# Optimization experiments

Measured on AMD Instinct MI355X. Metric: run time of the kernel, lower is better.

The kernel has to match this reference:

```python
import jax, jax.numpy as jnp
import numpy as np

D_MODEL = 1024
N_HEADS = 16
HEAD_DIM = D_MODEL // N_HEADS  # 64, rope_dim == head_dim
D_FF = 4096
BATCH = 2
SEQ = 2048
EPS = 1e-6


def setup_inputs() -> dict:
    key = jax.random.key(0)
    ks = jax.random.split(key, 12)
    x = jax.random.normal(ks[0], (BATCH, SEQ, D_MODEL), dtype=jnp.float32)
    # realistic RoPE angles: theta = pos * inv_freq, duplicated to fill rope_dim
    half = HEAD_DIM // 2
    inv_freq = 1.0 / (10000.0 ** (jnp.arange(0, half, dtype=jnp.float32) / half))
    pos = jnp.arange(SEQ, dtype=jnp.float32)
    freqs = pos[:, None] * inv_freq[None, :]              # [S, half]
    rotary_pos_emb = jnp.concatenate([freqs, freqs], axis=-1)[:, None, :]  # [S,1,64]
    s = D_MODEL ** -0.5
    wq = jax.random.normal(ks[1], (D_MODEL, D_MODEL), dtype=jnp.float32) * s
    wk = jax.random.normal(ks[2], (D_MODEL, D_MODEL), dtype=jnp.float32) * s
    wv = jax.random.normal(ks[3], (D_MODEL, D_MODEL), dtype=jnp.float32) * s
    wo = jax.random.normal(ks[4], (D_MODEL, D_MODEL), dtype=jnp.float32) * s
    w_gate = jax.random.normal(ks[5], (D_FF, D_MODEL), dtype=jnp.float32) * s
    w_up = jax.random.normal(ks[6], (D_FF, D_MODEL), dtype=jnp.float32) * s
    w_down = jax.random.normal(ks[7], (D_MODEL, D_FF), dtype=jnp.float32) * (D_FF ** -0.5)
    norm1_w = jnp.ones((D_MODEL,), dtype=jnp.float32)
    norm2_w = jnp.ones((D_MODEL,), dtype=jnp.float32)
    return {"x": x, "rotary_pos_emb": rotary_pos_emb, "wq": wq, "wk": wk,
            "wv": wv, "wo": wo, "w_gate": w_gate, "w_up": w_up,
            "w_down": w_down, "norm1_w": norm1_w, "norm2_w": norm2_w}


def _rms_norm(x, w):
    # torch: x / (||x||/sqrt(d) + eps) * w  (eps added to the norm, not variance)
    norm = jnp.linalg.norm(x, axis=-1, keepdims=True) * (x.shape[-1] ** -0.5)
    return x / (norm + EPS) * w


def _rotate_half(t):
    t1, t2 = jnp.split(t, 2, axis=-1)
    return jnp.concatenate([-t2, t1], axis=-1)


def _apply_rope(t, cos, sin):
    # t: [B,H,S,D]; cos/sin: [S,D] broadcast over batch/heads
    return t * cos[None, None] + _rotate_half(t) * sin[None, None]


def reference(x, rotary_pos_emb, wq, wk, wv, wo, w_gate, w_up, w_down, norm1_w, norm2_w):
    B, S, _ = x.shape
    H, D = N_HEADS, HEAD_DIM

    # ---- attention sublayer ----
    residual = x
    h = _rms_norm(x, norm1_w)
    q = (h @ wq.T).reshape(B, S, H, D).transpose(0, 2, 1, 3)  # [B,H,S,D]
    k = (h @ wk.T).reshape(B, S, H, D).transpose(0, 2, 1, 3)
    v = (h @ wv.T).reshape(B, S, H, D).transpose(0, 2, 1, 3)

    freqs = rotary_pos_emb[:, 0, :]  # [S, D] (rope_dim == head_dim)
    cos, sin = jnp.cos(freqs), jnp.sin(freqs)
    q = _apply_rope(q, cos, sin)
    k = _apply_rope(k, cos, sin)

    scores = jnp.einsum('bhsd,bhtd->bhst', q, k) / jnp.sqrt(jnp.float32(D))
    causal = jnp.tril(jnp.ones((S, S), dtype=bool))  # True = keep
    scores = jnp.where(causal[None, None], scores, jnp.finfo(scores.dtype).min)
    attn = jax.nn.softmax(scores, axis=-1)  # dropout is identity in eval
    attn_out = jnp.einsum('bhst,bhtd->bhsd', attn, v)
    attn_out = attn_out.transpose(0, 2, 1, 3).reshape(B, S, H * D)
    x = residual + attn_out @ wo.T

    # ---- SwiGLU MLP sublayer ----
    residual = x
    h = _rms_norm(x, norm2_w)
    gate = h @ w_gate.T
    up = h @ w_up.T
    ff = (jax.nn.silu(gate) * up) @ w_down.T
    return residual + ff
```

## Files before the change

### kernel.cpp

```cpp
#include <hip/hip_runtime.h>

typedef __bf16 bf16;
typedef __attribute__((ext_vector_type(8))) __bf16 bf16x8;
typedef __attribute__((ext_vector_type(4))) float f32x4;

#define B_SZ 2
#define SEQ 2048
#define DM 1024
#define NH 16
#define HD 64
#define DFF 4096
#define NROWS (B_SZ*SEQ)

__device__ __forceinline__ f32x4 mfma16(bf16x8 a, bf16x8 b, f32x4 c) {
    return __builtin_amdgcn_mfma_f32_16x16x32_bf16(a, b, c, 0, 0, 0);
}

__device__ __forceinline__ void gload16(const bf16* g, bf16* l) {
    __builtin_amdgcn_global_load_lds(
        (const __attribute__((address_space(1))) void*)g,
        (__attribute__((address_space(3))) void*)l, 16, 0, 0);
}


__global__ __launch_bounds__(256) void f32_to_bf16_k(const float* __restrict__ s,
                                                     bf16* __restrict__ d, int n) {
    int i = (blockIdx.x * 256 + threadIdx.x) * 4;
    int stride = gridDim.x * 1024;
    for (; i < n; i += stride) {
        float4 v = *(const float4*)(s + i);
        d[i]   = (bf16)v.x; d[i+1] = (bf16)v.y;
        d[i+2] = (bf16)v.z; d[i+3] = (bf16)v.w;
    }
}

__global__ __launch_bounds__(256) void conv_gu_k(const float* __restrict__ g,
                                                 const float* __restrict__ u,
                                                 bf16* __restrict__ d) {
    int i = (blockIdx.x * 256 + threadIdx.x) * 4;
    int fr = i >> 10, c = i & 1023;
    int b = fr >> 8, half = (fr >> 7) & 1, f = (b << 7) | (fr & 127);
    const float* src = (half ? u : g) + (long)f * 1024 + c;
    float4 v = *(const float4*)src;
    d[i]   = (bf16)v.x; d[i+1] = (bf16)v.y;
    d[i+2] = (bf16)v.z; d[i+3] = (bf16)v.w;
}

__global__ __launch_bounds__(256) void rope_table_k(const float* __restrict__ rope,
                                                    float* __restrict__ ct,
                                                    float* __restrict__ st) {
    int i = blockIdx.x * 256 + threadIdx.x;
    int sI = i >> 5, d = i & 31;
    float f = rope[sI * 64 + d];
    ct[i] = cosf(f);
    st[i] = sinf(f);
}

__global__ __launch_bounds__(256) void rmsnorm_k(const float* __restrict__ x,
                                                 const float* __restrict__ w,
                                                 bf16* __restrict__ o) {
    int row = blockIdx.x;
    int tid = threadIdx.x;
    float4 v = ((const float4*)(x + (long)row * DM))[tid];
    float ss = v.x*v.x + v.y*v.y + v.z*v.z + v.w*v.w;
    #pragma unroll
    for (int off = 32; off >= 1; off >>= 1) ss += __shfl_xor(ss, off, 64);
    __shared__ float sred[4];
    if ((tid & 63) == 0) sred[tid >> 6] = ss;
    __syncthreads();
    float tot = sred[0] + sred[1] + sred[2] + sred[3];
    float scale = 1.f / (sqrtf(tot * (1.f / (float)DM)) + 1e-6f);
    float4 wv = ((const float4*)w)[tid];
    bf16* orow = o + (long)row * DM + tid * 4;
    orow[0] = (bf16)(v.x * scale * wv.x);
    orow[1] = (bf16)(v.y * scale * wv.y);
    orow[2] = (bf16)(v.z * scale * wv.z);
    orow[3] = (bf16)(v.w * scale * wv.w);
}


template<int EPI>
__global__ __launch_bounds__(512, 2)
void gemm256(const bf16* __restrict__ A, const bf16* __restrict__ W,
             int K, bf16* __restrict__ o1, bf16* __restrict__ o2,
             bf16* __restrict__ o3,
             const float* __restrict__ ct, const float* __restrict__ st) {
    __shared__ __align__(16) char smem[131072];
    const int tid = threadIdx.x;
    const int wid = tid >> 6, l = tid & 63;
    const int lr = l & 15, lg = l >> 4;
    const int wr = wid >> 1, wc = wid & 1;
    const int nwg = gridDim.x * gridDim.y;
    const int orig = blockIdx.y * gridDim.x + blockIdx.x;
    const int swz = (orig & 7) * (nwg >> 3) + (orig >> 3);
    const int bx = swz % gridDim.x, by = swz / gridDim.x;
    const long mbase = (long)bx * 256;
    const long nbase = (long)by * 256;

    f32x4 acc[4][8] = {};
    const int nk = K >> 6;

    auto stage = [&](int b, int kt) {
        bf16* bufA = (bf16*)(smem + b * 65536);
        bf16* bufB = (bf16*)(smem + b * 65536 + 32768);
        #pragma unroll
        for (int i = 0; i < 4; ++i) {
            int s = i * 512 + tid;
            int row = s >> 3, c8 = (s & 7) << 3;
            gload16(&A[(mbase + row) * K + kt * 64 + c8], bufA + s * 8);
            gload16(&W[(nbase + row) * K + kt * 64 + c8], bufB + s * 8);
        }
    };
    auto compute = [&](int b) {
        const bf16* bufA = (const bf16*)(smem + b * 65536);
        const bf16* bufB = (const bf16*)(smem + b * 65536 + 32768);
        #pragma unroll
        for (int kk = 0; kk < 2; ++kk) {
            bf16x8 af[4], bfr[8];
            #pragma unroll
            for (int mi = 0; mi < 4; ++mi)
                af[mi] = *(const bf16x8*)&bufA[(wr * 64 + mi * 16 + lr) * 64 + kk * 32 + lg * 8];
            #pragma unroll
            for (int ni = 0; ni < 8; ++ni)
                bfr[ni] = *(const bf16x8*)&bufB[(wc * 128 + ni * 16 + lr) * 64 + kk * 32 + lg * 8];
            #pragma unroll
            for (int mi = 0; mi < 4; ++mi)
                #pragma unroll
                for (int ni = 0; ni < 8; ++ni)
                    acc[mi][ni] = mfma16(af[mi], bfr[ni], acc[mi][ni]);
        }
    };

    stage(0, 0);
    __syncthreads();
    int cur = 0;
    for (int kt = 0; kt < nk - 1; ++kt) {
        stage(cur ^ 1, kt + 1);
        compute(cur);
        __syncthreads();
        cur ^= 1;
    }
    compute(cur);

    if (EPI == 0) {
        const long colW = nbase + wc * 128;
        const int sect = (int)(colW >> 10);
        #pragma unroll
        for (int mi = 0; mi < 4; ++mi) {
            #pragma unroll
            for (int nn = 0; nn < 4; ++nn) {
                const int ni = (nn & 1) + (nn >> 1) * 4;
                const int col = (int)colW + ni * 16 + lr;
                const int h = (col >> 6) & 15;
                const int d = col & 31;
                #pragma unroll
                for (int r = 0; r < 4; ++r) {
                    long row = mbase + wr * 64 + mi * 16 + 4 * lg + r;
                    int b = (int)(row >> 11), s = (int)(row & 2047);
                    float v1 = acc[mi][ni][r];
                    float v2 = acc[mi][ni + 2][r];
                    if (sect < 2) {
                        float c = ct[s * 32 + d], sn = st[s * 32 + d];
                        bf16* dst = (sect == 0) ? o1 : o2;
                        long p = (((long)(b * NH + h) * SEQ + s) << 6) + d;
                        dst[p]      = (bf16)(v1 * c - v2 * sn);
                        dst[p + 32] = (bf16)(v2 * c + v1 * sn);
                    } else {
                        long p = ((long)(b * NH + h) * HD + d) * SEQ + s;
                        o3[p]            = (bf16)v1;
                        o3[p + 32 * SEQ] = (bf16)v2;
                    }
                }
            }
        }
    }

    if (EPI == 3) {
        const int fbase = (int)(nbase >> 1);
        bf16* Gl = (bf16*)smem;
        __syncthreads();
        if (wc == 0) {
            #pragma unroll
            for (int mi = 0; mi < 4; ++mi)
                #pragma unroll
                for (int ni = 0; ni < 8; ++ni)
                    #pragma unroll
                    for (int r = 0; r < 4; ++r) {
                        int grow = wr * 64 + mi * 16 + 4 * lg + r;
                        Gl[grow * 132 + ni * 16 + lr] = (bf16)acc[mi][ni][r];
                    }
        }
        __syncthreads();
        if (wc == 1) {
            #pragma unroll
            for (int mi = 0; mi < 4; ++mi)
                #pragma unroll
                for (int ni = 0; ni < 8; ++ni)
                    #pragma unroll
                    for (int r = 0; r < 4; ++r) {
                        int grow = wr * 64 + mi * 16 + 4 * lg + r;
                        float g = (float)Gl[grow * 132 + ni * 16 + lr];
                        float u = acc[mi][ni][r];
                        float sg = g / (1.f + __expf(-g));
                        long row = mbase + grow;
                        o1[row * 4096 + fbase + ni * 16 + lr] = (bf16)(sg * u);
                    }
        }
    }
}


__global__ __launch_bounds__(512, 4)
void gemm64x128(const bf16* __restrict__ A, const bf16* __restrict__ W,
                int K, int N, const float* __restrict__ resid, float* __restrict__ of) {
    __shared__ bf16 As[2][64 * 64];
    __shared__ bf16 Bs[2][128 * 64];
    const int tid = threadIdx.x;
    const int wid = tid >> 6, l = tid & 63;
    const int lr = l & 15, lg = l >> 4;
    const int wr = wid >> 2, wcn = wid & 3;
    const long mbase = (long)blockIdx.x * 64;
    const long nbase = (long)blockIdx.y * 128;

    f32x4 acc[2][2] = {};
    const int nk = K >> 6;

    auto stage = [&](int b, int kt) {
        {
            int s = tid;
            int row = s >> 3, c8 = (s & 7) << 3;
            gload16(&A[(mbase + row) * K + kt * 64 + c8], &As[b][s * 8]);
        }
        #pragma unroll
        for (int i = 0; i < 2; ++i) {
            int s = i * 512 + tid;
            int row = s >> 3, c8 = (s & 7) << 3;
            gload16(&W[(nbase + row) * K + kt * 64 + c8], &Bs[b][s * 8]);
        }
    };
    auto compute = [&](int b) {
        #pragma unroll
        for (int kk = 0; kk < 2; ++kk) {
            bf16x8 af[2], bfr[2];
            #pragma unroll
            for (int mi = 0; mi < 2; ++mi)
                af[mi] = *(const bf16x8*)&As[b][(wr * 32 + mi * 16 + lr) * 64 + kk * 32 + lg * 8];
            #pragma unroll
            for (int ni = 0; ni < 2; ++ni)
                bfr[ni] = *(const bf16x8*)&Bs[b][(wcn * 32 + ni * 16 + lr) * 64 + kk * 32 + lg * 8];
            #pragma unroll
            for (int mi = 0; mi < 2; ++mi)
                #pragma unroll
                for (int ni = 0; ni < 2; ++ni)
                    acc[mi][ni] = mfma16(af[mi], bfr[ni], acc[mi][ni]);
        }
    };

    stage(0, 0);
    __syncthreads();
    int cur = 0;
    for (int kt = 0; kt < nk - 1; ++kt) {
        stage(cur ^ 1, kt + 1);
        compute(cur);
        __syncthreads();
        cur ^= 1;
    }
    compute(cur);

    #pragma unroll
    for (int mi = 0; mi < 2; ++mi)
        #pragma unroll
        for (int ni = 0; ni < 2; ++ni)
            #pragma unroll
            for (int r = 0; r < 4; ++r) {
                long row = mbase + wr * 32 + mi * 16 + 4 * lg + r;
                long col = nbase + wcn * 32 + ni * 16 + lr;
                of[row * N + col] = resid[row * N + col] + acc[mi][ni][r];
            }
}


__device__ __forceinline__ void attn_tile(
    int tb, int qw, bool diag,
    const bf16x8& qf0, const bf16x8& qf1,
    const bf16* Kl, const bf16* Vl, bf16* Plw,
    int lr, int lg, f32x4* oacc, float* mr, f32x4& lacc)
{
    f32x4 s[4];
    __builtin_amdgcn_s_setprio(1);
    #pragma unroll
    for (int tf = 0; tf < 4; ++tf) {
        f32x4 z = {0.f, 0.f, 0.f, 0.f};
        bf16x8 k0 = *(const bf16x8*)&Kl[(tf * 16 + lr) * 64 + ((0 + lg) ^ (lr & 7)) * 8];
        bf16x8 k1 = *(const bf16x8*)&Kl[(tf * 16 + lr) * 64 + ((4 + lg) ^ (lr & 7)) * 8];
        z = mfma16(qf0, k0, z);
        z = mfma16(qf1, k1, z);
        s[tf] = z;
    }
    __builtin_amdgcn_s_setprio(0);

    float pv[4][4];
    float pmax[4] = {-1e30f, -1e30f, -1e30f, -1e30f};
    #pragma unroll
    for (int tf = 0; tf < 4; ++tf) {
        int t = tb + tf * 16 + lr;
        #pragma unroll
        for (int r = 0; r < 4; ++r) {
            float sv = s[tf][r] * 0.125f;
            if (diag && t > qw + 4 * lg + r) sv = -1e30f;
            pv[tf][r] = sv;
            pmax[r] = fmaxf(pmax[r], sv);
        }
    }
    #pragma unroll
    for (int r = 0; r < 4; ++r) {
        pmax[r] = fmaxf(pmax[r], __shfl_xor(pmax[r], 8, 64));
        pmax[r] = fmaxf(pmax[r], __shfl_xor(pmax[r], 4, 64));
        pmax[r] = fmaxf(pmax[r], __shfl_xor(pmax[r], 2, 64));
        pmax[r] = fmaxf(pmax[r], __shfl_xor(pmax[r], 1, 64));
    }
    float alpha[4];
    #pragma unroll
    for (int r = 0; r < 4; ++r) {
        float mn = fmaxf(mr[r], pmax[r]);
        alpha[r] = __expf(mr[r] - mn);
        mr[r] = mn;
    }
    #pragma unroll
    for (int tf = 0; tf < 4; ++tf)
        #pragma unroll
        for (int r = 0; r < 4; ++r)
            Plw[(4 * lg + r) * 68 + tf * 16 + lr] = (bf16)__expf(pv[tf][r] - mr[r]);

    #pragma unroll
    for (int r = 0; r < 4; ++r) lacc[r] *= alpha[r];
    #pragma unroll
    for (int df = 0; df < 4; ++df) {
        f32x4 t4 = oacc[df];
        t4[0] *= alpha[0]; t4[1] *= alpha[1];
        t4[2] *= alpha[2]; t4[3] *= alpha[3];
        oacc[df] = t4;
    }
    bf16x8 pa0, pa1;
    #pragma unroll
    for (int j = 0; j < 8; ++j) {
        pa0[j] = Plw[lr * 68 + lg * 8 + j];
        pa1[j] = Plw[lr * 68 + 32 + lg * 8 + j];
    }
    bf16x8 ones;
    #pragma unroll
    for (int j = 0; j < 8; ++j) ones[j] = (bf16)1.0f;
    __builtin_amdgcn_s_setprio(1);
    lacc = mfma16(pa0, ones, lacc);
    lacc = mfma16(pa1, ones, lacc);
    #pragma unroll
    for (int df = 0; df < 4; ++df) {
        bf16x8 v0 = *(const bf16x8*)&Vl[(df * 16 + lr) * 64 + ((0 + lg) ^ (lr & 7)) * 8];
        bf16x8 v1 = *(const bf16x8*)&Vl[(df * 16 + lr) * 64 + ((4 + lg) ^ (lr & 7)) * 8];
        oacc[df] = mfma16(pa0, v0, oacc[df]);
        oacc[df] = mfma16(pa1, v1, oacc[df]);
    }
    __builtin_amdgcn_s_setprio(0);
}

__global__ __launch_bounds__(256)
void attn_fwd(const bf16* __restrict__ q, const bf16* __restrict__ k,
              const bf16* __restrict__ vt, bf16* __restrict__ o) {
    __shared__ bf16 Kl[2][64 * 64];
    __shared__ bf16 Vl[2][64 * 64];
    __shared__ bf16 Pl[4][16 * 68];
    const int tid = threadIdx.x, wid = tid >> 6, l = tid & 63;
    const int lr = l & 15, lg = l >> 4;
    const int qtA = blockIdx.x;
    const int qtB = 31 - qtA;
    const int bh = blockIdx.y;
    const long kbase = (long)bh * SEQ * HD;
    const long vbase = (long)bh * HD * SEQ;
    const int qwA = qtA * 64 + wid * 16;
    const int qwB = qtB * 64 + wid * 16;

    bf16x8 qA0, qA1, qB0, qB1;
    {
        const bf16* qp = q + kbase + (long)(qwA + lr) * HD + lg * 8;
        qA0 = *(const bf16x8*)qp; qA1 = *(const bf16x8*)(qp + 32);
        const bf16* qp2 = q + kbase + (long)(qwB + lr) * HD + lg * 8;
        qB0 = *(const bf16x8*)qp2; qB1 = *(const bf16x8*)(qp2 + 32);
    }
    f32x4 oA[4] = {}, oB[4] = {};
    f32x4 lA = {0.f, 0.f, 0.f, 0.f}, lB = {0.f, 0.f, 0.f, 0.f};
    float mA[4] = {-1e30f, -1e30f, -1e30f, -1e30f};
    float mB[4] = {-1e30f, -1e30f, -1e30f, -1e30f};

    auto stageKV = [&](int b, int tb) {
        #pragma unroll
        for (int i = 0; i < 4; ++i) {
            int slot = i * 256 + tid;
            int row = (slot >> 3) & 63;
            int bs = (slot & 7) ^ (row & 7);
            if (slot < 512)
                gload16(&k[kbase + (long)(tb + row) * HD + bs * 8], &Kl[b][slot * 8]);
            else
                gload16(&vt[vbase + (long)row * SEQ + tb + bs * 8], &Vl[b][(slot - 512) * 8]);
        }
    };

    const int nt = qtB + 1;
    stageKV(0, 0);
    __syncthreads();
    int cur = 0;
    for (int tb_i = 0; tb_i < nt; ++tb_i) {
        const int tb = tb_i * 64;
        if (tb_i + 1 < nt) stageKV(cur ^ 1, tb + 64);
        if (tb_i <= qtA)
            attn_tile(tb, qwA, tb_i == qtA, qA0, qA1, Kl[cur], Vl[cur], Pl[wid], lr, lg, oA, mA, lA);
        attn_tile(tb, qwB, tb_i == qtB, qB0, qB1, Kl[cur], Vl[cur], Pl[wid], lr, lg, oB, mB, lB);
        __syncthreads();
        cur ^= 1;
    }

    const int b = bh >> 4, h = bh & 15;
    #pragma unroll
    for (int df = 0; df < 4; ++df) {
        #pragma unroll
        for (int r = 0; r < 4; ++r) {
            int sA = qwA + 4 * lg + r;
            int sB = qwB + 4 * lg + r;
            o[((long)(b * SEQ + sA) * DM) + h * HD + df * 16 + lr] = (bf16)(oA[df][r] / lA[r]);
            o[((long)(b * SEQ + sB) * DM) + h * HD + df * 16 + lr] = (bf16)(oB[df][r] / lB[r]);
        }
    }
}


extern "C" void kernel_launch(void* const* d_in, const int* in_sizes, int n_in,
                              void* d_out, int out_size, void* d_ws, size_t ws_size,
                              hipStream_t stream) {
    (void)in_sizes; (void)n_in; (void)out_size; (void)ws_size;
    const float* x    = (const float*)d_in[0];
    const float* rope = (const float*)d_in[1];
    const float* wq   = (const float*)d_in[2];
    const float* wk   = (const float*)d_in[3];
    const float* wv   = (const float*)d_in[4];
    const float* wo   = (const float*)d_in[5];
    const float* wg   = (const float*)d_in[6];
    const float* wu   = (const float*)d_in[7];
    const float* wd   = (const float*)d_in[8];
    const float* n1w  = (const float*)d_in[9];
    const float* n2w  = (const float*)d_in[10];
    float* out = (float*)d_out;

    char* ws = (char*)d_ws;
    const size_t MB = 1u << 20;
    bf16* wqkvb = (bf16*)(ws + 0 * MB);
    bf16* wob   = (bf16*)(ws + 6 * MB);
    bf16* wgub  = (bf16*)(ws + 8 * MB);
    bf16* wdb   = (bf16*)(ws + 24 * MB);
    bf16* hb    = (bf16*)(ws + 32 * MB);
    bf16* qb_   = (bf16*)(ws + 40 * MB);
    bf16* kb_   = (bf16*)(ws + 56 * MB);
    bf16* vtb   = (bf16*)(ws + 72 * MB);
    bf16* attnb = (bf16*)(ws + 88 * MB);
    float* x2   = (float*)(ws + 40 * MB);
    bf16* midb  = (bf16*)(ws + 56 * MB);
    float* ctab = (float*)(ws + 104 * MB);
    float* stab = (float*)(ws + 104 * MB + (1u << 18));

    f32_to_bf16_k<<<1024, 256, 0, stream>>>(wq, wqkvb,               DM * DM);
    f32_to_bf16_k<<<1024, 256, 0, stream>>>(wk, wqkvb + 1024 * 1024, DM * DM);
    f32_to_bf16_k<<<1024, 256, 0, stream>>>(wv, wqkvb + 2048 * 1024, DM * DM);
    f32_to_bf16_k<<<1024, 256, 0, stream>>>(wo, wob, DM * DM);
    conv_gu_k<<<8192, 256, 0, stream>>>(wg, wu, wgub);
    f32_to_bf16_k<<<2048, 256, 0, stream>>>(wd, wdb, DM * DFF);
    rope_table_k<<<256, 256, 0, stream>>>(rope, ctab, stab);

    rmsnorm_k<<<NROWS, 256, 0, stream>>>(x, n1w, hb);

    gemm256<0><<<dim3(16, 12), 512, 0, stream>>>(hb, wqkvb, DM, qb_, kb_, vtb, ctab, stab);

    attn_fwd<<<dim3(16, 32), 256, 0, stream>>>(qb_, kb_, vtb, attnb);

    gemm64x128<<<dim3(64, 8), 512, 0, stream>>>(attnb, wob, DM, DM, x, x2);

    rmsnorm_k<<<NROWS, 256, 0, stream>>>(x2, n2w, hb);

    gemm256<3><<<dim3(16, 32), 512, 0, stream>>>(hb, wgub, DM, midb, nullptr, nullptr, nullptr, nullptr);

    gemm64x128<<<dim3(64, 8), 512, 0, stream>>>(midb, wdb, DFF, DM, x2, out);
}
```

Before: 353.8 us.

## Fuse weight conversions and deepen gemm256 pipeline with swizzled half-K stages

Merges six weight-conversion launches into one kernel that converts eight elements per thread. Reworks the 256x256 GEMM to stage half K-tiles (32 columns) into a four-deep ring in LDS with an XOR swizzle. It waits on explicit vmcnt counts plus a raw s_barrier instead of __syncthreads, and raises wave priority around the MFMA bursts. The warp layout changes from 4x2 to 2x4 waves, so the RoPE and SwiGLU epilogues are remapped. This aims to hide load latency and cut LDS bank conflicts, at the cost of fragile hand-written wait counts and synchronisation.

```diff
diff --git a/kernel.cpp b/kernel.cpp
--- a/kernel.cpp
+++ b/kernel.cpp
@@ -23,27 +23,34 @@
 }
 
 
-__global__ __launch_bounds__(256) void f32_to_bf16_k(const float* __restrict__ s,
-                                                     bf16* __restrict__ d, int n) {
-    int i = (blockIdx.x * 256 + threadIdx.x) * 4;
-    int stride = gridDim.x * 1024;
-    for (; i < n; i += stride) {
-        float4 v = *(const float4*)(s + i);
-        d[i]   = (bf16)v.x; d[i+1] = (bf16)v.y;
-        d[i+2] = (bf16)v.z; d[i+3] = (bf16)v.w;
-    }
-}
-
-__global__ __launch_bounds__(256) void conv_gu_k(const float* __restrict__ g,
-                                                 const float* __restrict__ u,
-                                                 bf16* __restrict__ d) {
-    int i = (blockIdx.x * 256 + threadIdx.x) * 4;
-    int fr = i >> 10, c = i & 1023;
-    int b = fr >> 8, half = (fr >> 7) & 1, f = (b << 7) | (fr & 127);
-    const float* src = (half ? u : g) + (long)f * 1024 + c;
-    float4 v = *(const float4*)src;
-    d[i]   = (bf16)v.x; d[i+1] = (bf16)v.y;
-    d[i+2] = (bf16)v.z; d[i+3] = (bf16)v.w;
+__global__ __launch_bounds__(256) void convert_all_k(
+    const float* __restrict__ wq, const float* __restrict__ wk,
+    const float* __restrict__ wv, const float* __restrict__ wo,
+    const float* __restrict__ wg, const float* __restrict__ wu,
+    const float* __restrict__ wd,
+    bf16* __restrict__ wqkvb, bf16* __restrict__ wob,
+    bf16* __restrict__ wgub, bf16* __restrict__ wdb) {
+    const long M1 = 1l << 20;
+    long i = ((long)blockIdx.x * 256 + threadIdx.x) * 8;
+    const float* src; bf16* dst; long off;
+    if (i < 3 * M1) {
+        int sct = (int)(i >> 20);
+        src = sct == 0 ? wq : (sct == 1 ? wk : wv);
+        off = i & (M1 - 1); dst = wqkvb + i;
+    } else if (i < 4 * M1) {
+        src = wo; off = i - 3 * M1; dst = wob + off;
+    } else if (i < 12 * M1) {
+        long j = i - 4 * M1;
+        int fr = (int)(j >> 10), c = (int)(j & 1023);
+        int b = fr >> 8, half = (fr >> 7) & 1, f = (b << 7) | (fr & 127);
+        src = half ? wu : wg; off = (long)f * 1024 + c; dst = wgub + j;
+    } else {
+        src = wd; off = i - 12 * M1; dst = wdb + off;
+    }
+    float4 v0 = *(const float4*)(src + off);
+    float4 v1 = *(const float4*)(src + off + 4);
+    dst[0] = (bf16)v0.x; dst[1] = (bf16)v0.y; dst[2] = (bf16)v0.z; dst[3] = (bf16)v0.w;
+    dst[4] = (bf16)v1.x; dst[5] = (bf16)v1.y; dst[6] = (bf16)v1.z; dst[7] = (bf16)v1.w;
 }
 
 __global__ __launch_bounds__(256) void rope_table_k(const float* __restrict__ rope,
@@ -86,10 +93,12 @@
              bf16* __restrict__ o3,
              const float* __restrict__ ct, const float* __restrict__ st) {
     __shared__ __align__(16) char smem[131072];
+    bf16* Ah = (bf16*)smem;
+    bf16* Bh = (bf16*)(smem + 65536);
     const int tid = threadIdx.x;
     const int wid = tid >> 6, l = tid & 63;
     const int lr = l & 15, lg = l >> 4;
-    const int wr = wid >> 1, wc = wid & 1;
+    const int wr = wid >> 2, wcn = wid & 3;
     const int nwg = gridDim.x * gridDim.y;
     const int orig = blockIdx.y * gridDim.x + blockIdx.x;
     const int swz = (orig & 7) * (nwg >> 3) + (orig >> 3);
@@ -97,78 +106,91 @@
     const long mbase = (long)bx * 256;
     const long nbase = (long)by * 256;
 
-    f32x4 acc[4][8] = {};
+    f32x4 acc[8][4] = {};
     const int nk = K >> 6;
-
-    auto stage = [&](int b, int kt) {
-        bf16* bufA = (bf16*)(smem + b * 65536);
-        bf16* bufB = (bf16*)(smem + b * 65536 + 32768);
-        #pragma unroll
-        for (int i = 0; i < 4; ++i) {
+    const int P = nk * 2;
+
+    const int aoff0 = lr * 64 + ((wr * 4 + lg) ^ (lr & 7)) * 8;
+    const int boff0 = ((wcn & 1) * 64 + lr) * 64 + (((wcn >> 1) * 4 + lg) ^ (lr & 7)) * 8;
+
+    auto stageHalf = [&](int ph) {
+        const int d = (ph >> 1) & 1, h = ph & 1, kt = ph >> 1;
+        bf16* abase = Ah + (d * 2 + h) * 8192;
+        bf16* bbase = Bh + (d * 2 + h) * 8192;
+        const long kcol = (long)kt * 64 + h * 32;
+        #pragma unroll
+        for (int i = 0; i < 2; ++i) {
             int s = i * 512 + tid;
-            int row = s >> 3, c8 = (s & 7) << 3;
-            gload16(&A[(mbase + row) * K + kt * 64 + c8], bufA + s * 8);
-            gload16(&W[(nbase + row) * K + kt * 64 + c8], bufB + s * 8);
+            int prow = s >> 3, pblk = s & 7;
+            int L = pblk ^ (prow & 7);
+            long gr = (long)((L >> 2) * 128 + prow);
+            long gc = kcol + (L & 3) * 8;
+            gload16(&A[(mbase + gr) * K + gc], abase + s * 8);
+            gload16(&W[(nbase + gr) * K + gc], bbase + s * 8);
         }
     };
-    auto compute = [&](int b) {
-        const bf16* bufA = (const bf16*)(smem + b * 65536);
-        const bf16* bufB = (const bf16*)(smem + b * 65536 + 32768);
-        #pragma unroll
-        for (int kk = 0; kk < 2; ++kk) {
-            bf16x8 af[4], bfr[8];
+
+    auto computeHalf = [&](int ph) {
+        const int d = (ph >> 1) & 1, h = ph & 1;
+        const bf16* abase = Ah + (d * 2 + h) * 8192;
+        const bf16* bbase = Bh + (d * 2 + h) * 8192;
+        bf16x8 bfr[4];
+        #pragma unroll
+        for (int ni = 0; ni < 4; ++ni)
+            bfr[ni] = *(const bf16x8*)&bbase[ni * 1024 + boff0];
+        #pragma unroll
+        for (int ms = 0; ms < 2; ++ms) {
+            bf16x8 af[4];
             #pragma unroll
             for (int mi = 0; mi < 4; ++mi)
-                af[mi] = *(const bf16x8*)&bufA[(wr * 64 + mi * 16 + lr) * 64 + kk * 32 + lg * 8];
-            #pragma unroll
-            for (int ni = 0; ni < 8; ++ni)
-                bfr[ni] = *(const bf16x8*)&bufB[(wc * 128 + ni * 16 + lr) * 64 + kk * 32 + lg * 8];
+                af[mi] = *(const bf16x8*)&abase[(ms * 4 + mi) * 1024 + aoff0];
+            __builtin_amdgcn_s_setprio(1);
             #pragma unroll
             for (int mi = 0; mi < 4; ++mi)
                 #pragma unroll
-                for (int ni = 0; ni < 8; ++ni)
-                    acc[mi][ni] = mfma16(af[mi], bfr[ni], acc[mi][ni]);
+                for (int ni = 0; ni < 4; ++ni)
+                    acc[ms * 4 + mi][ni] = mfma16(af[mi], bfr[ni], acc[ms * 4 + mi][ni]);
+            __builtin_amdgcn_s_setprio(0);
         }
     };
 
-    stage(0, 0);
-    __syncthreads();
-    int cur = 0;
-    for (int kt = 0; kt < nk - 1; ++kt) {
-        stage(cur ^ 1, kt + 1);
-        compute(cur);
-        __syncthreads();
-        cur ^= 1;
-    }
-    compute(cur);
+    stageHalf(0);
+    stageHalf(1);
+    for (int p = 0; p < P; ++p) {
+        if (p + 2 < P) stageHalf(p + 2);
+        if (p < P - 2)       asm volatile("s_waitcnt vmcnt(8)" ::: "memory");
+        else if (p == P - 2) asm volatile("s_waitcnt vmcnt(4)" ::: "memory");
+        else                 asm volatile("s_waitcnt vmcnt(0)" ::: "memory");
+        __builtin_amdgcn_s_barrier();
+        __builtin_amdgcn_sched_barrier(0);
+        computeHalf(p);
+    }
 
     if (EPI == 0) {
-        const long colW = nbase + wc * 128;
+        const long colW = nbase + wcn * 64;
         const int sect = (int)(colW >> 10);
-        #pragma unroll
-        for (int mi = 0; mi < 4; ++mi) {
-            #pragma unroll
-            for (int nn = 0; nn < 4; ++nn) {
-                const int ni = (nn & 1) + (nn >> 1) * 4;
-                const int col = (int)colW + ni * 16 + lr;
-                const int h = (col >> 6) & 15;
-                const int d = col & 31;
+        const int hh = (int)((colW >> 6) & 15);
+        #pragma unroll
+        for (int a = 0; a < 8; ++a) {
+            #pragma unroll
+            for (int nn = 0; nn < 2; ++nn) {
+                const int dd = nn * 16 + lr;
                 #pragma unroll
                 for (int r = 0; r < 4; ++r) {
-                    long row = mbase + wr * 64 + mi * 16 + 4 * lg + r;
+                    long row = mbase + wr * 128 + a * 16 + 4 * lg + r;
                     int b = (int)(row >> 11), s = (int)(row & 2047);
-                    float v1 = acc[mi][ni][r];
-                    float v2 = acc[mi][ni + 2][r];
+                    float v1 = acc[a][nn][r];
+                    float v2 = acc[a][nn + 2][r];
                     if (sect < 2) {
-                        float c = ct[s * 32 + d], sn = st[s * 32 + d];
+                        float c = ct[s * 32 + dd], sn = st[s * 32 + dd];
                         bf16* dst = (sect == 0) ? o1 : o2;
-                        long p = (((long)(b * NH + h) * SEQ + s) << 6) + d;
-                        dst[p]      = (bf16)(v1 * c - v2 * sn);
-                        dst[p + 32] = (bf16)(v2 * c + v1 * sn);
+                        long pth = (((long)(b * NH + hh) * SEQ + s) << 6) + dd;
+                        dst[pth]      = (bf16)(v1 * c - v2 * sn);
+                        dst[pth + 32] = (bf16)(v2 * c + v1 * sn);
                     } else {
-                        long p = ((long)(b * NH + h) * HD + d) * SEQ + s;
-                        o3[p]            = (bf16)v1;
-                        o3[p + 32 * SEQ] = (bf16)v2;
+                        long pth = ((long)(b * NH + hh) * HD + dd) * SEQ + s;
+                        o3[pth]            = (bf16)v1;
+                        o3[pth + 32 * SEQ] = (bf16)v2;
                     }
                 }
             }
@@ -179,31 +201,33 @@
         const int fbase = (int)(nbase >> 1);
         bf16* Gl = (bf16*)smem;
         __syncthreads();
-        if (wc == 0) {
-            #pragma unroll
-            for (int mi = 0; mi < 4; ++mi)
+        if (wcn < 2) {
+            #pragma unroll
+            for (int a = 0; a < 8; ++a)
                 #pragma unroll
-                for (int ni = 0; ni < 8; ++ni)
+                for (int ni = 0; ni < 4; ++ni)
                     #pragma unroll
                     for (int r = 0; r < 4; ++r) {
-                        int grow = wr * 64 + mi * 16 + 4 * lg + r;
-                        Gl[grow * 132 + ni * 16 + lr] = (bf16)acc[mi][ni][r];
+                        int grow = wr * 128 + a * 16 + 4 * lg + r;
+                        int fc = wcn * 64 + ni * 16 + lr;
+                        Gl[grow * 132 + fc] = (bf16)acc[a][ni][r];
                     }
         }
         __syncthreads();
-        if (wc == 1) {
-            #pragma unroll
-            for (int mi = 0; mi < 4; ++mi)
+        if (wcn >= 2) {
+            #pragma unroll
+            for (int a = 0; a < 8; ++a)
                 #pragma unroll
-                for (int ni = 0; ni < 8; ++ni)
+                for (int ni = 0; ni < 4; ++ni)
                     #pragma unroll
                     for (int r = 0; r < 4; ++r) {
-                        int grow = wr * 64 + mi * 16 + 4 * lg + r;
-                        float g = (float)Gl[grow * 132 + ni * 16 + lr];
-                        float u = acc[mi][ni][r];
+                        int grow = wr * 128 + a * 16 + 4 * lg + r;
+                        int fc = (wcn - 2) * 64 + ni * 16 + lr;
+                        float g = (float)Gl[grow * 132 + fc];
+                        float u = acc[a][ni][r];
                         float sg = g / (1.f + __expf(-g));
                         long row = mbase + grow;
-                        o1[row * 4096 + fbase + ni * 16 + lr] = (bf16)(sg * u);
+                        o1[row * 4096 + fbase + fc] = (bf16)(sg * u);
                     }
         }
     }
@@ -465,12 +489,8 @@
     float* ctab = (float*)(ws + 104 * MB);
     float* stab = (float*)(ws + 104 * MB + (1u << 18));
 
-    f32_to_bf16_k<<<1024, 256, 0, stream>>>(wq, wqkvb,               DM * DM);
-    f32_to_bf16_k<<<1024, 256, 0, stream>>>(wk, wqkvb + 1024 * 1024, DM * DM);
-    f32_to_bf16_k<<<1024, 256, 0, stream>>>(wv, wqkvb + 2048 * 1024, DM * DM);
-    f32_to_bf16_k<<<1024, 256, 0, stream>>>(wo, wob, DM * DM);
-    conv_gu_k<<<8192, 256, 0, stream>>>(wg, wu, wgub);
-    f32_to_bf16_k<<<2048, 256, 0, stream>>>(wd, wdb, DM * DFF);
+    convert_all_k<<<8192, 256, 0, stream>>>(wq, wk, wv, wo, wg, wu, wd,
+                                            wqkvb, wob, wgub, wdb);
     rope_table_k<<<256, 256, 0, stream>>>(rope, ctab, stab);
 
     rmsnorm_k<<<NROWS, 256, 0, stream>>>(x, n1w, hb);
```

Result: faster. 331.8 us (-6.2%).
